# Kernel optimization log

Measured on AMD Instinct MI355X. Metric: run time of the kernel, lower is better.

The kernel has to match this reference:

```python
import jax, jax.numpy as jnp
import numpy as np

EMBED_DIM = 1024
SHIFT = 0.0

def setup_inputs() -> dict:
    key = jax.random.key(0)
    k1, k2, k3 = jax.random.split(key, 3)
    inputs = jax.random.normal(k1, (4, 2048, EMBED_DIM), dtype=jnp.float32)
    rotation_params = jax.random.normal(k2, (EMBED_DIM, EMBED_DIM), dtype=jnp.float32)
    entangle_params = jax.random.normal(k3, (EMBED_DIM, EMBED_DIM), dtype=jnp.float32)
    return {"inputs": inputs, "rotation_params": rotation_params, "entangle_params": entangle_params}

def reference(inputs, rotation_params, entangle_params):
    # inputs: (b, s, d)
    d = inputs.shape[-1]
    query = jnp.einsum('bsd,de->bse', inputs, rotation_params)
    key = jnp.einsum('bsd,de->bse', inputs, entangle_params)
    scores = jax.nn.softmax(jnp.einsum('bqd,bkd->bqk', query, key) / np.sqrt(d), axis=-1)
    out = jnp.einsum('bqk,bkd->bqd', scores, inputs)
    return jax.nn.sigmoid(out + SHIFT)
```

## Files before the change

### kernel.cpp

```cpp
#include <hip/hip_runtime.h>
#include <hip/hip_bf16.h>
#include <math.h>


using u16 = unsigned short;
using short8 = __attribute__((ext_vector_type(8))) short;
using f32x4  = __attribute__((ext_vector_type(4))) float;

#define MFB(a, b, c) __builtin_amdgcn_mfma_f32_16x16x32_bf16((a), (b), (c), 0, 0, 0)

__device__ static inline u16 f2bf(float f) {
    union { __hip_bfloat16 h; u16 u; } cv; cv.h = __float2bfloat16(f); return cv.u;
}
__device__ static inline float bf2f(u16 u) {
    union { __hip_bfloat16 h; u16 u; } cv; cv.u = u; return __bfloat162float(cv.h);
}
__device__ static inline void split2(float v, u16& h, u16& l) {
    h = f2bf(v);
    l = f2bf(v - bf2f(h));
}

__device__ static inline void gload16(const u16* g, u16* l) {
    __builtin_amdgcn_global_load_lds(
        (const __attribute__((address_space(1))) void*)g,
        (__attribute__((address_space(3))) void*)l, 16, 0, 0);
}

__device__ static inline short8 ldfrag(const u16* sm, int row, int g) {
    const int off = row * 32 + ((g ^ ((row >> 1) & 3)) << 3);
    return *reinterpret_cast<const short8*>(sm + off);
}

enum { EP_F32 = 0, EP_HILO = 1, EP_SIG = 2 };

template<int EPI, bool TRIPLE>
__global__ __launch_bounds__(256)
void gemm_split(const u16* __restrict__ Ahi, const u16* __restrict__ Alo,
                const u16* __restrict__ Bhi, const u16* __restrict__ Blo,
                float* __restrict__ Cf, u16* __restrict__ Chi, u16* __restrict__ Clo,
                int K, int lda, int ldb, int ldc,
                long sA, long sB, long sC, float alpha)
{
    const int z = blockIdx.z;
    Ahi += z * sA;
    Bhi += z * sB;
    if (TRIPLE) { Alo += z * sA; Blo += z * sB; }
    if (EPI == EP_HILO) { Chi += z * sC; Clo += z * sC; }
    else                { Cf  += z * sC; }

    constexpr int BUFSZ  = TRIPLE ? 16384 : 8192;
    constexpr int OFF_BH = TRIPLE ? 8192 : 4096;
    __shared__ __align__(16) u16 smem[2 * BUFSZ];

    const int t = threadIdx.x;
    const int wave = t >> 6, lane = t & 63;
    const int row0 = blockIdx.y * 128, col0 = blockIdx.x * 128;

    const int rr = t >> 2, cc = t & 3;
    const int gg = cc ^ ((rr >> 1) & 3);
    const u16* gAh = Ahi + (long)(row0 + rr) * lda + gg * 8;
    const u16* gBh = Bhi + (long)(col0 + rr) * ldb + gg * 8;
    const u16* gAl = TRIPLE ? (Alo + (long)(row0 + rr) * lda + gg * 8) : nullptr;
    const u16* gBl = TRIPLE ? (Blo + (long)(col0 + rr) * ldb + gg * 8) : nullptr;
    const long a2 = (long)64 * lda, b2 = (long)64 * ldb;

    f32x4 acc[4][4];
    #pragma unroll
    for (int m = 0; m < 4; m++)
        #pragma unroll
        for (int n = 0; n < 4; n++)
            acc[m][n] = (f32x4){0.f, 0.f, 0.f, 0.f};

    const int lr = lane & 15, lg = lane >> 4;
    const int wm = (wave >> 1) * 64, wn = (wave & 1) * 64;
    const int NT = K >> 5;

    {
        u16* d = smem + t * 8;
        gload16(gAh,      d);
        gload16(gAh + a2, d + 2048);
        gload16(gBh,      d + OFF_BH);
        gload16(gBh + b2, d + OFF_BH + 2048);
        if (TRIPLE) {
            gload16(gAl,      d + 4096);
            gload16(gAl + a2, d + 4096 + 2048);
            gload16(gBl,      d + 12288);
            gload16(gBl + b2, d + 12288 + 2048);
        }
    }

    for (int tk = 0; tk < NT; ++tk) {
        __syncthreads();
        const u16* sb = smem + (tk & 1) * BUFSZ;
        if (tk + 1 < NT) {
            const int kn = (tk + 1) << 5;
            u16* d = smem + ((tk + 1) & 1) * BUFSZ + t * 8;
            gload16(gAh + kn,      d);
            gload16(gAh + kn + a2, d + 2048);
            gload16(gBh + kn,      d + OFF_BH);
            gload16(gBh + kn + b2, d + OFF_BH + 2048);
            if (TRIPLE) {
                gload16(gAl + kn,      d + 4096);
                gload16(gAl + kn + a2, d + 4096 + 2048);
                gload16(gBl + kn,      d + 12288);
                gload16(gBl + kn + b2, d + 12288 + 2048);
            }
        }
        const u16* sAh = sb;
        const u16* sAl = sb + 4096;
        const u16* sBh = sb + OFF_BH;
        const u16* sBl = sb + 12288;

        short8 bh[4], bl[4], ah[4], al[4];
        #pragma unroll
        for (int n = 0; n < 4; n++) {
            bh[n] = ldfrag(sBh, wn + n * 16 + lr, lg);
            if (TRIPLE) bl[n] = ldfrag(sBl, wn + n * 16 + lr, lg);
        }
        #pragma unroll
        for (int m = 0; m < 4; m++) {
            ah[m] = ldfrag(sAh, wm + m * 16 + lr, lg);
            if (TRIPLE) al[m] = ldfrag(sAl, wm + m * 16 + lr, lg);
        }
        __builtin_amdgcn_s_setprio(1);
        #pragma unroll
        for (int m = 0; m < 4; m++) {
            #pragma unroll
            for (int n = 0; n < 4; n++) {
                acc[m][n] = MFB(ah[m], bh[n], acc[m][n]);
                if (TRIPLE) {
                    acc[m][n] = MFB(ah[m], bl[n], acc[m][n]);
                    acc[m][n] = MFB(al[m], bh[n], acc[m][n]);
                }
            }
        }
        __builtin_amdgcn_s_setprio(0);
    }

    #pragma unroll
    for (int m = 0; m < 4; m++) {
        #pragma unroll
        for (int n = 0; n < 4; n++) {
            #pragma unroll
            for (int r = 0; r < 4; r++) {
                const int grow = row0 + wm + m * 16 + lg * 4 + r;
                const int gcol = col0 + wn + n * 16 + lr;
                const float v = alpha * acc[m][n][r];
                const long o = (long)grow * ldc + gcol;
                if (EPI == EP_F32) {
                    Cf[o] = v;
                } else if (EPI == EP_SIG) {
                    Cf[o] = 1.0f / (1.0f + __expf(-v));
                } else {
                    u16 h, l; split2(v, h, l);
                    Chi[o] = h; Clo[o] = l;
                }
            }
        }
    }
}

__global__ __launch_bounds__(1024)
void gemm_triple_256(const u16* __restrict__ Ahi, const u16* __restrict__ Alo,
                     const u16* __restrict__ Bhi, const u16* __restrict__ Blo,
                     float* __restrict__ Cf,
                     int K, int lda, int ldb, int ldc,
                     long sA, long sB, long sC, float alpha)
{
    const int z = blockIdx.z;
    Ahi += z * sA; Alo += z * sA;
    Bhi += z * sB; Blo += z * sB;
    Cf  += z * sC;

    __shared__ __align__(16) u16 smem[65536];

    const int t = threadIdx.x;
    const int wave = t >> 6, lane = t & 63;
    const int lr = lane & 15, lg = lane >> 4;

    const int u = blockIdx.x + 8 * blockIdx.y;
    const int reg = u & 7, j = u >> 3;
    const int bx = 2 * (reg & 3) + (j & 1);
    const int by = 4 * (reg >> 2) + (j >> 1);
    const int row0 = by * 256, col0 = bx * 256;
    const int wm = (wave >> 2) * 64, wn = (wave & 3) * 64;

    const int srow = t >> 2;
    const int sg = (t & 3) ^ ((srow >> 1) & 3);
    const u16* gAh = Ahi + (long)(row0 + srow) * lda + sg * 8;
    const u16* gAl = Alo + (long)(row0 + srow) * lda + sg * 8;
    const u16* gBh = Bhi + (long)(col0 + srow) * ldb + sg * 8;
    const u16* gBl = Blo + (long)(col0 + srow) * ldb + sg * 8;

    f32x4 acc[4][4];
    #pragma unroll
    for (int m = 0; m < 4; m++)
        #pragma unroll
        for (int n = 0; n < 4; n++)
            acc[m][n] = (f32x4){0.f, 0.f, 0.f, 0.f};

    const int NT = K >> 5;

    {
        u16* d = smem + t * 8;
        gload16(gAh, d);
        gload16(gAl, d + 8192);
        gload16(gBh, d + 16384);
        gload16(gBl, d + 24576);
    }

    for (int tk = 0; tk < NT; ++tk) {
        __syncthreads();
        const u16* sb = smem + (tk & 1) * 32768;
        if (tk + 1 < NT) {
            const int kn = (tk + 1) << 5;
            u16* d = smem + ((tk + 1) & 1) * 32768 + t * 8;
            gload16(gAh + kn, d);
            gload16(gAl + kn, d + 8192);
            gload16(gBh + kn, d + 16384);
            gload16(gBl + kn, d + 24576);
        }
        const u16* sAh = sb;
        const u16* sAl = sb + 8192;
        const u16* sBh = sb + 16384;
        const u16* sBl = sb + 24576;

        short8 bh[4], bl[4];
        #pragma unroll
        for (int n = 0; n < 4; n++) {
            bh[n] = ldfrag(sBh, wn + n * 16 + lr, lg);
            bl[n] = ldfrag(sBl, wn + n * 16 + lr, lg);
        }
        __builtin_amdgcn_s_setprio(1);
        #pragma unroll
        for (int m = 0; m < 4; m++) {
            const short8 ah = ldfrag(sAh, wm + m * 16 + lr, lg);
            const short8 al = ldfrag(sAl, wm + m * 16 + lr, lg);
            #pragma unroll
            for (int n = 0; n < 4; n++) {
                acc[m][n] = MFB(ah, bh[n], acc[m][n]);
                acc[m][n] = MFB(ah, bl[n], acc[m][n]);
                acc[m][n] = MFB(al, bh[n], acc[m][n]);
            }
        }
        __builtin_amdgcn_s_setprio(0);
    }

    #pragma unroll
    for (int m = 0; m < 4; m++) {
        #pragma unroll
        for (int n = 0; n < 4; n++) {
            #pragma unroll
            for (int r = 0; r < 4; r++) {
                const int grow = row0 + wm + m * 16 + lg * 4 + r;
                const int gcol = col0 + wn + n * 16 + lr;
                Cf[(long)grow * ldc + gcol] = alpha * acc[m][n][r];
            }
        }
    }
}

__global__ __launch_bounds__(256)
void split_rm3(const float* __restrict__ in0, u16* __restrict__ hi0, u16* __restrict__ lo0, long n0,
               const float* __restrict__ in1, u16* __restrict__ hi1, u16* __restrict__ lo1, long n1,
               const float* __restrict__ in2, u16* __restrict__ hi2, u16* __restrict__ lo2)
{
    long i = ((long)blockIdx.x * 256 + threadIdx.x) * 4;
    const float* in; u16 *hi, *lo;
    if (i < n0)           { in = in0; hi = hi0; lo = lo0; }
    else if (i < n0 + n1) { i -= n0; in = in1; hi = hi1; lo = lo1; }
    else                  { i -= n0 + n1; in = in2; hi = hi2; lo = lo2; }
    const float4 v = *reinterpret_cast<const float4*>(in + i);
    ushort4 h, l;
    split2(v.x, h.x, l.x);
    split2(v.y, h.y, l.y);
    split2(v.z, h.z, l.z);
    split2(v.w, h.w, l.w);
    *reinterpret_cast<ushort4*>(hi + i) = h;
    *reinterpret_cast<ushort4*>(lo + i) = l;
}

__global__ __launch_bounds__(256)
void reduce4_split(const float* __restrict__ p, u16* __restrict__ hi, u16* __restrict__ lo,
                   long n)
{
    const long i = ((long)blockIdx.x * 256 + threadIdx.x) * 4;
    const float4 a = *reinterpret_cast<const float4*>(p + i);
    const float4 b = *reinterpret_cast<const float4*>(p + n + i);
    const float4 c = *reinterpret_cast<const float4*>(p + 2 * n + i);
    const float4 d = *reinterpret_cast<const float4*>(p + 3 * n + i);
    ushort4 h, l;
    split2((a.x + b.x) + (c.x + d.x), h.x, l.x);
    split2((a.y + b.y) + (c.y + d.y), h.y, l.y);
    split2((a.z + b.z) + (c.z + d.z), h.z, l.z);
    split2((a.w + b.w) + (c.w + d.w), h.w, l.w);
    *reinterpret_cast<ushort4*>(hi + i) = h;
    *reinterpret_cast<ushort4*>(lo + i) = l;
}

template<bool HILO>
__global__ __launch_bounds__(256)
void split_tr(const float* __restrict__ in, u16* __restrict__ hi, u16* __restrict__ lo,
              int R, int C, long sIn, long sOut)
{
    in += (long)blockIdx.z * sIn;
    hi += (long)blockIdx.z * sOut;
    if (HILO) lo += (long)blockIdx.z * sOut;

    __shared__ float tile[32][33];
    const int tx = threadIdx.x & 31, ty = threadIdx.x >> 5;
    const int r0 = blockIdx.y * 32, c0 = blockIdx.x * 32;

    #pragma unroll
    for (int j = 0; j < 4; j++)
        tile[ty * 4 + j][tx] = in[(long)(r0 + ty * 4 + j) * C + c0 + tx];
    __syncthreads();

    #pragma unroll
    for (int j = 0; j < 4; j++) {
        const int oc = ty * 4 + j;
        const float v = tile[tx][oc];
        u16 h, l; split2(v, h, l);
        const long o = (long)(c0 + oc) * R + r0 + tx;
        hi[o] = h;
        if (HILO) lo[o] = l;
    }
}

__global__ __launch_bounds__(256)
void softmax_hi(const float* __restrict__ S, u16* __restrict__ hi)
{
    const int NC = 2048;
    const long base = (long)blockIdx.x * NC;
    const float* p = S + base;
    const int tid = threadIdx.x;

    float4 v0 = reinterpret_cast<const float4*>(p)[tid];
    float4 v1 = reinterpret_cast<const float4*>(p)[tid + 256];

    float m = fmaxf(fmaxf(fmaxf(v0.x, v0.y), fmaxf(v0.z, v0.w)),
                    fmaxf(fmaxf(v1.x, v1.y), fmaxf(v1.z, v1.w)));
    #pragma unroll
    for (int off = 1; off < 64; off <<= 1)
        m = fmaxf(m, __shfl_xor(m, off));

    __shared__ float redm[4];
    __shared__ float reds[4];
    const int wave = tid >> 6, lane = tid & 63;
    if (lane == 0) redm[wave] = m;
    __syncthreads();
    m = fmaxf(fmaxf(redm[0], redm[1]), fmaxf(redm[2], redm[3]));

    v0.x = __expf(v0.x - m); v0.y = __expf(v0.y - m);
    v0.z = __expf(v0.z - m); v0.w = __expf(v0.w - m);
    v1.x = __expf(v1.x - m); v1.y = __expf(v1.y - m);
    v1.z = __expf(v1.z - m); v1.w = __expf(v1.w - m);

    float s = (v0.x + v0.y + v0.z + v0.w) + (v1.x + v1.y + v1.z + v1.w);
    #pragma unroll
    for (int off = 1; off < 64; off <<= 1)
        s += __shfl_xor(s, off);
    if (lane == 0) reds[wave] = s;
    __syncthreads();
    s = (reds[0] + reds[1]) + (reds[2] + reds[3]);

    const float inv = 1.0f / s;
    ushort4 h0, h1;
    h0.x = f2bf(v0.x * inv); h0.y = f2bf(v0.y * inv);
    h0.z = f2bf(v0.z * inv); h0.w = f2bf(v0.w * inv);
    h1.x = f2bf(v1.x * inv); h1.y = f2bf(v1.y * inv);
    h1.z = f2bf(v1.z * inv); h1.w = f2bf(v1.w * inv);

    reinterpret_cast<ushort4*>(hi + base)[tid]       = h0;
    reinterpret_cast<ushort4*>(hi + base)[tid + 256] = h1;
}

extern "C" void kernel_launch(void* const* d_in, const int* in_sizes, int n_in,
                              void* d_out, int out_size, void* d_ws, size_t ws_size,
                              hipStream_t stream)
{
    (void)in_sizes; (void)n_in; (void)out_size; (void)ws_size;
    const float* X = (const float*)d_in[0];
    const float* R = (const float*)d_in[1];
    const float* E = (const float*)d_in[2];
    float* out = (float*)d_out;

    const int B = 4, SQ = 2048, D = 1024;
    const long NDX = (long)B * SQ * D;
    const long DD  = (long)D * D;
    const long SS  = (long)B * SQ * SQ;
    const long M16 = 8388608;

    u16* wsu = (u16*)d_ws;
    u16* Xhi  = wsu;
    u16* Xlo  = Xhi + NDX;
    u16* Rhi  = wsu + 2 * M16;
    u16* Rlo  = Rhi + DD;
    u16* Ehi  = Rlo + DD;
    u16* Elo  = Ehi + DD;
    u16* Yhi  = wsu + 2 * M16;
    u16* Ylo  = Yhi + NDX;
    u16* Shi  = wsu + 2 * M16;
    u16* Xthi = wsu;
    float* Wpart = (float*)(wsu + 4 * M16);
    u16* Wthi = wsu + 5 * M16;
    u16* Wtlo = Wthi + DD;
    float* Sf = (float*)(wsu + 4 * M16);

    dim3 thr(256);

    split_rm3<<<dim3((unsigned)((NDX + 2 * DD) / 1024)), thr, 0, stream>>>(
        X, Xhi, Xlo, NDX, R, Rhi, Rlo, DD, E, Ehi, Elo);

    gemm_split<EP_F32, true><<<dim3(D / 128, D / 128, 4), thr, 0, stream>>>(
        Ehi, Elo, Rhi, Rlo, Wpart, nullptr, nullptr,
        256, D, D, D, 256, 256, DD, 1.0f);
    reduce4_split<<<dim3((unsigned)(DD / 1024)), thr, 0, stream>>>(Wpart, Wthi, Wtlo, DD);

    gemm_split<EP_HILO, true><<<dim3(D / 128, (B * SQ) / 128, 1), thr, 0, stream>>>(
        Xhi, Xlo, Wthi, Wtlo, nullptr, Yhi, Ylo,
        D, D, D, D, 0, 0, 0, 1.0f);

    gemm_triple_256<<<dim3(SQ / 256, SQ / 256, B), dim3(1024), 0, stream>>>(
        Yhi, Ylo, Xhi, Xlo, Sf,
        D, D, D, SQ,
        (long)SQ * D, (long)SQ * D, (long)SQ * SQ, 0.03125f);

    softmax_hi<<<dim3(B * SQ), thr, 0, stream>>>(Sf, Shi);

    split_tr<false><<<dim3(D / 32, SQ / 32, B), thr, 0, stream>>>(
        X, Xthi, nullptr, SQ, D, (long)SQ * D, (long)SQ * D);

    gemm_split<EP_SIG, false><<<dim3(D / 128, SQ / 128, B), thr, 0, stream>>>(
        Shi, nullptr, Xthi, nullptr, out, nullptr, nullptr,
        SQ, SQ, SQ, D,
        (long)SQ * SQ, (long)SQ * D, (long)SQ * D, 1.0f);
}
```

Baseline: 242.5 us.

## Drop split-K for weight product and deepen K tile in final GEMM

The gemm_split kernel gains a KH template parameter that stages several 32-wide K slices per pipeline step, halving the barrier count. The final scores×X GEMM uses KH=2. The 1024x1024 weight-product GEMM no longer uses a 4-way split-K with a separate reduction kernel. It now runs as a single 64-block launch that writes hi/lo output directly, removing one launch and the partial-sum traffic but lowering parallelism for that step.

```diff
diff --git a/kernel.cpp b/kernel.cpp
--- a/kernel.cpp
+++ b/kernel.cpp
@@ -33,7 +33,7 @@
 
 enum { EP_F32 = 0, EP_HILO = 1, EP_SIG = 2 };
 
-template<int EPI, bool TRIPLE>
+template<int EPI, bool TRIPLE, int KH>
 __global__ __launch_bounds__(256)
 void gemm_split(const u16* __restrict__ Ahi, const u16* __restrict__ Alo,
                 const u16* __restrict__ Bhi, const u16* __restrict__ Blo,
@@ -48,8 +48,8 @@
     if (EPI == EP_HILO) { Chi += z * sC; Clo += z * sC; }
     else                { Cf  += z * sC; }
 
-    constexpr int BUFSZ  = TRIPLE ? 16384 : 8192;
-    constexpr int OFF_BH = TRIPLE ? 8192 : 4096;
+    constexpr int AUNIT = TRIPLE ? 8192 : 4096;
+    constexpr int BUFSZ = KH * 2 * AUNIT;
     __shared__ __align__(16) u16 smem[2 * BUFSZ];
 
     const int t = threadIdx.x;
@@ -64,6 +64,26 @@
     const u16* gBl = TRIPLE ? (Blo + (long)(col0 + rr) * ldb + gg * 8) : nullptr;
     const long a2 = (long)64 * lda, b2 = (long)64 * ldb;
 
+    auto STAGE = [&](int buf, int k0) {
+        u16* base = smem + buf * BUFSZ + t * 8;
+        #pragma unroll
+        for (int kh = 0; kh < KH; kh++) {
+            const int kk = k0 + kh * 32;
+            u16* dA = base + kh * AUNIT;
+            u16* dB = base + KH * AUNIT + kh * AUNIT;
+            gload16(gAh + kk,      dA);
+            gload16(gAh + kk + a2, dA + 2048);
+            gload16(gBh + kk,      dB);
+            gload16(gBh + kk + b2, dB + 2048);
+            if (TRIPLE) {
+                gload16(gAl + kk,      dA + 4096);
+                gload16(gAl + kk + a2, dA + 6144);
+                gload16(gBl + kk,      dB + 4096);
+                gload16(gBl + kk + b2, dB + 6144);
+            }
+        }
+    };
+
     f32x4 acc[4][4];
     #pragma unroll
     for (int m = 0; m < 4; m++)
@@ -73,68 +93,47 @@
 
     const int lr = lane & 15, lg = lane >> 4;
     const int wm = (wave >> 1) * 64, wn = (wave & 1) * 64;
-    const int NT = K >> 5;
-
-    {
-        u16* d = smem + t * 8;
-        gload16(gAh,      d);
-        gload16(gAh + a2, d + 2048);
-        gload16(gBh,      d + OFF_BH);
-        gload16(gBh + b2, d + OFF_BH + 2048);
-        if (TRIPLE) {
-            gload16(gAl,      d + 4096);
-            gload16(gAl + a2, d + 4096 + 2048);
-            gload16(gBl,      d + 12288);
-            gload16(gBl + b2, d + 12288 + 2048);
-        }
-    }
+    const int NT = K / (32 * KH);
+
+    STAGE(0, 0);
 
     for (int tk = 0; tk < NT; ++tk) {
         __syncthreads();
         const u16* sb = smem + (tk & 1) * BUFSZ;
-        if (tk + 1 < NT) {
-            const int kn = (tk + 1) << 5;
-            u16* d = smem + ((tk + 1) & 1) * BUFSZ + t * 8;
-            gload16(gAh + kn,      d);
-            gload16(gAh + kn + a2, d + 2048);
-            gload16(gBh + kn,      d + OFF_BH);
-            gload16(gBh + kn + b2, d + OFF_BH + 2048);
-            if (TRIPLE) {
-                gload16(gAl + kn,      d + 4096);
-                gload16(gAl + kn + a2, d + 4096 + 2048);
-                gload16(gBl + kn,      d + 12288);
-                gload16(gBl + kn + b2, d + 12288 + 2048);
-            }
-        }
-        const u16* sAh = sb;
-        const u16* sAl = sb + 4096;
-        const u16* sBh = sb + OFF_BH;
-        const u16* sBl = sb + 12288;
-
-        short8 bh[4], bl[4], ah[4], al[4];
-        #pragma unroll
-        for (int n = 0; n < 4; n++) {
-            bh[n] = ldfrag(sBh, wn + n * 16 + lr, lg);
-            if (TRIPLE) bl[n] = ldfrag(sBl, wn + n * 16 + lr, lg);
-        }
-        #pragma unroll
-        for (int m = 0; m < 4; m++) {
-            ah[m] = ldfrag(sAh, wm + m * 16 + lr, lg);
-            if (TRIPLE) al[m] = ldfrag(sAl, wm + m * 16 + lr, lg);
-        }
-        __builtin_amdgcn_s_setprio(1);
-        #pragma unroll
-        for (int m = 0; m < 4; m++) {
+        if (tk + 1 < NT) STAGE((tk + 1) & 1, (tk + 1) * 32 * KH);
+
+        #pragma unroll
+        for (int kh = 0; kh < KH; kh++) {
+            const u16* sAh = sb + kh * AUNIT;
+            const u16* sAl = sAh + 4096;
+            const u16* sBh = sb + KH * AUNIT + kh * AUNIT;
+            const u16* sBl = sBh + 4096;
+
+            short8 bh[4], bl[4], ah[4], al[4];
             #pragma unroll
             for (int n = 0; n < 4; n++) {
-                acc[m][n] = MFB(ah[m], bh[n], acc[m][n]);
-                if (TRIPLE) {
-                    acc[m][n] = MFB(ah[m], bl[n], acc[m][n]);
-                    acc[m][n] = MFB(al[m], bh[n], acc[m][n]);
+                bh[n] = ldfrag(sBh, wn + n * 16 + lr, lg);
+                if (TRIPLE) bl[n] = ldfrag(sBl, wn + n * 16 + lr, lg);
+            }
+            #pragma unroll
+            for (int m = 0; m < 4; m++) {
+                ah[m] = ldfrag(sAh, wm + m * 16 + lr, lg);
+                if (TRIPLE) al[m] = ldfrag(sAl, wm + m * 16 + lr, lg);
+            }
+            __builtin_amdgcn_s_setprio(1);
+            #pragma unroll
+            for (int m = 0; m < 4; m++) {
+                #pragma unroll
+                for (int n = 0; n < 4; n++) {
+                    acc[m][n] = MFB(ah[m], bh[n], acc[m][n]);
+                    if (TRIPLE) {
+                        acc[m][n] = MFB(ah[m], bl[n], acc[m][n]);
+                        acc[m][n] = MFB(al[m], bh[n], acc[m][n]);
+                    }
                 }
             }
-        }
-        __builtin_amdgcn_s_setprio(0);
+            __builtin_amdgcn_s_setprio(0);
+        }
     }
 
     #pragma unroll
@@ -280,24 +279,6 @@
     *reinterpret_cast<ushort4*>(lo + i) = l;
 }
 
-__global__ __launch_bounds__(256)
-void reduce4_split(const float* __restrict__ p, u16* __restrict__ hi, u16* __restrict__ lo,
-                   long n)
-{
-    const long i = ((long)blockIdx.x * 256 + threadIdx.x) * 4;
-    const float4 a = *reinterpret_cast<const float4*>(p + i);
-    const float4 b = *reinterpret_cast<const float4*>(p + n + i);
-    const float4 c = *reinterpret_cast<const float4*>(p + 2 * n + i);
-    const float4 d = *reinterpret_cast<const float4*>(p + 3 * n + i);
-    ushort4 h, l;
-    split2((a.x + b.x) + (c.x + d.x), h.x, l.x);
-    split2((a.y + b.y) + (c.y + d.y), h.y, l.y);
-    split2((a.z + b.z) + (c.z + d.z), h.z, l.z);
-    split2((a.w + b.w) + (c.w + d.w), h.w, l.w);
-    *reinterpret_cast<ushort4*>(hi + i) = h;
-    *reinterpret_cast<ushort4*>(lo + i) = l;
-}
-
 template<bool HILO>
 __global__ __launch_bounds__(256)
 void split_tr(const float* __restrict__ in, u16* __restrict__ hi, u16* __restrict__ lo,
@@ -402,7 +383,6 @@
     u16* Ylo  = Yhi + NDX;
     u16* Shi  = wsu + 2 * M16;
     u16* Xthi = wsu;
-    float* Wpart = (float*)(wsu + 4 * M16);
     u16* Wthi = wsu + 5 * M16;
     u16* Wtlo = Wthi + DD;
     float* Sf = (float*)(wsu + 4 * M16);
@@ -412,12 +392,11 @@
     split_rm3<<<dim3((unsigned)((NDX + 2 * DD) / 1024)), thr, 0, stream>>>(
         X, Xhi, Xlo, NDX, R, Rhi, Rlo, DD, E, Ehi, Elo);
 
-    gemm_split<EP_F32, true><<<dim3(D / 128, D / 128, 4), thr, 0, stream>>>(
-        Ehi, Elo, Rhi, Rlo, Wpart, nullptr, nullptr,
-        256, D, D, D, 256, 256, DD, 1.0f);
-    reduce4_split<<<dim3((unsigned)(DD / 1024)), thr, 0, stream>>>(Wpart, Wthi, Wtlo, DD);
-
-    gemm_split<EP_HILO, true><<<dim3(D / 128, (B * SQ) / 128, 1), thr, 0, stream>>>(
+    gemm_split<EP_HILO, true, 1><<<dim3(D / 128, D / 128, 1), thr, 0, stream>>>(
+        Ehi, Elo, Rhi, Rlo, nullptr, Wthi, Wtlo,
+        D, D, D, D, 0, 0, 0, 1.0f);
+
+    gemm_split<EP_HILO, true, 1><<<dim3(D / 128, (B * SQ) / 128, 1), thr, 0, stream>>>(
         Xhi, Xlo, Wthi, Wtlo, nullptr, Yhi, Ylo,
         D, D, D, D, 0, 0, 0, 1.0f);
 
@@ -431,7 +410,7 @@
     split_tr<false><<<dim3(D / 32, SQ / 32, B), thr, 0, stream>>>(
         X, Xthi, nullptr, SQ, D, (long)SQ * D, (long)SQ * D);
 
-    gemm_split<EP_SIG, false><<<dim3(D / 128, SQ / 128, B), thr, 0, stream>>>(
+    gemm_split<EP_SIG, false, 2><<<dim3(D / 128, SQ / 128, B), thr, 0, stream>>>(
         Shi, nullptr, Xthi, nullptr, out, nullptr, nullptr,
         SQ, SQ, SQ, D,
         (long)SQ * SQ, (long)SQ * D, (long)SQ * D, 1.0f);
```

New measurement: 250.2 us. 1.03x slower.
